# Optimization experiments

Measured on AMD Instinct MI355X. Metric: run time of the kernel, lower is better.

Reference implementation:

```python
import math
import jax, jax.numpy as jnp
import numpy as np

DIM, NHEAD, TOPK = 1024, 16, 64
DK = DIM // NHEAD
HIDDEN = int(DIM * 8.0)
EPS = 1e-5


def setup_inputs() -> dict:
    key = jax.random.key(0)
    ks = jax.random.split(key, 12)
    B, T = 2, 2048
    s = 0.02
    return {
        "x": jax.random.normal(ks[0], (B, T, DIM), jnp.float32),
        "ln1_g": jnp.ones((DIM,), jnp.float32),
        "ln1_b": jnp.zeros((DIM,), jnp.float32),
        "w_qkv": jax.random.normal(ks[1], (DIM, 3 * DIM), jnp.float32) * s,
        "alpha_head": jnp.zeros((NHEAD,), jnp.float32),
        "w_out": jax.random.normal(ks[2], (DIM, DIM), jnp.float32) * s,
        "ln2_g": jnp.ones((DIM,), jnp.float32),
        "ln2_b": jnp.zeros((DIM,), jnp.float32),
        "w1": jax.random.normal(ks[3], (DIM, HIDDEN), jnp.float32) * s,
        "b1": jnp.zeros((HIDDEN,), jnp.float32),
        "w2": jax.random.normal(ks[4], (HIDDEN, DIM), jnp.float32) * s,
        "b2": jnp.zeros((DIM,), jnp.float32),
        "alpha": jnp.float32(0.5),
    }


def _layernorm(x, g, b):
    mu = jnp.mean(x, axis=-1, keepdims=True)
    var = jnp.var(x, axis=-1, keepdims=True)
    return (x - mu) * jax.lax.rsqrt(var + EPS) * g + b


def _adaptive_sparse_attn(xn, w_qkv, alpha_head, w_out):
    B, T, C = xn.shape
    qkv = xn @ w_qkv  # [B,T,3C]
    q, k, v = jnp.split(qkv, 3, axis=-1)
    def heads(t):
        return t.reshape(B, T, NHEAD, DK).transpose(0, 2, 1, 3)  # [B,H,T,dk]
    q, k, v = heads(q), heads(k), heads(v)
    attn = jnp.einsum("bhqd,bhkd->bhqk", q, k) / math.sqrt(DK)  # [B,H,T,T]
    dense = jnp.einsum("bhqk,bhkd->bhqd", jax.nn.softmax(attn, axis=-1), v)
    # top-k sparse branch (TOPK < T)
    _, idx = jax.lax.top_k(attn, TOPK)  # [B,H,T,TOPK]
    M = B * NHEAD * T
    keep = jnp.zeros((M, T), bool).at[jnp.arange(M)[:, None], idx.reshape(M, TOPK)].set(True)
    keep = keep.reshape(B, NHEAD, T, T)
    attn_sp = jnp.where(keep, attn, jnp.float32(-1e9))
    sparse = jnp.einsum("bhqk,bhkd->bhqd", jax.nn.softmax(attn_sp, axis=-1), v)
    gate = jax.nn.sigmoid(alpha_head)[None, :, None, None]
    out = gate * dense + (1.0 - gate) * sparse  # [B,H,T,dk]
    out = out.transpose(0, 2, 1, 3).reshape(B, T, C)
    return out @ w_out


def reference(x, ln1_g, ln1_b, w_qkv, alpha_head, w_out, ln2_g, ln2_b, w1, b1, w2, b2, alpha):
    # attention sub-block with learned residual scale alpha
    x = x + alpha * _adaptive_sparse_attn(_layernorm(x, ln1_g, ln1_b), w_qkv, alpha_head, w_out)
    # FFN (dropout in eval mode -> identity); exact GELU as torch default
    h = jax.nn.gelu(_layernorm(x, ln2_g, ln2_b) @ w1 + b1, approximate=False)
    x = x + alpha * (h @ w2 + b2)
    return x
```

## Files before the change

### kernel.cpp

```cpp
#include <hip/hip_runtime.h>
#include <hip/hip_bf16.h>
#include <math.h>

#define DIMC 1024
#define NHEADC 16
#define DKC 64
#define HIDC 8192
#define TSEQ 2048
#define BATCH 2
#define NROWS (BATCH*TSEQ)
#define EPSF 1e-5f

typedef __attribute__((ext_vector_type(8))) short short8;
typedef __attribute__((ext_vector_type(4))) float floatx4;

__device__ __forceinline__ unsigned pk2bf(float a, float b){
  float2 t; t.x = a; t.y = b;
  __hip_bfloat162 h = __float22bfloat162_rn(t);
  union { __hip_bfloat162 h; unsigned u; } cv; cv.h = h;
  return cv.u;
}
__device__ __forceinline__ ushort f2bf(float f){
  return (ushort)(pk2bf(f, f) & 0xFFFFu);
}
__device__ __forceinline__ floatx4 mfma16(short8 a, short8 b, floatx4 c){
  return __builtin_amdgcn_mfma_f32_16x16x32_bf16(a, b, c, 0, 0, 0);
}
__device__ __forceinline__ void gld_lds16(const void* g, void* l){
  __builtin_amdgcn_global_load_lds((const __attribute__((address_space(1))) unsigned*)g,
                                   (__attribute__((address_space(3))) unsigned*)l, 16, 0, 0);
}
__device__ __forceinline__ float wred_add(float v){
  #pragma unroll
  for (int o = 32; o > 0; o >>= 1) v += __shfl_xor(v, o, 64);
  return v;
}
__device__ __forceinline__ int wred_addi(int v){
  #pragma unroll
  for (int o = 32; o > 0; o >>= 1) v += __shfl_xor(v, o, 64);
  return v;
}
__device__ __forceinline__ unsigned wred_maxu(unsigned v){
  #pragma unroll
  for (int o = 32; o > 0; o >>= 1) { unsigned w = __shfl_xor((int)v, o, 64); v = v > w ? v : w; }
  return v;
}
__device__ __forceinline__ unsigned wred_minu(unsigned v){
  #pragma unroll
  for (int o = 32; o > 0; o >>= 1) { unsigned w = __shfl_xor((int)v, o, 64); v = v < w ? v : w; }
  return v;
}
__device__ __forceinline__ float lo16f(unsigned u){ return __uint_as_float(u << 16); }
__device__ __forceinline__ float hi16f(unsigned u){ return __uint_as_float(u & 0xFFFF0000u); }
__device__ __forceinline__ unsigned pk2key(unsigned u){
  const unsigned s = u & 0x80008000u;
  return u ^ (0x80008000u | (s - (s >> 15)));
}
__device__ __forceinline__ unsigned key2pk(unsigned k){
  const unsigned s = k & 0x80008000u;
  return k ^ ~(s - (s >> 15));
}

__global__ __launch_bounds__(256)
void wconv_t(const float* __restrict__ W, ushort* __restrict__ WT, int K, int N)
{
  __shared__ float tile[32][33];
  const int t = threadIdx.x, tx = t & 31, ty = t >> 5;
  const int n0 = blockIdx.x * 32, k0 = blockIdx.y * 32;
  #pragma unroll
  for (int r = 0; r < 4; ++r)
    tile[ty + r*8][tx] = W[(size_t)(k0 + ty + r*8) * N + n0 + tx];
  __syncthreads();
  #pragma unroll
  for (int r = 0; r < 4; ++r)
    WT[(size_t)(n0 + ty + r*8) * K + k0 + tx] = f2bf(tile[tx][ty + r*8]);
}

__global__ __launch_bounds__(256)
void vtrans(const ushort* __restrict__ qkv, ushort* __restrict__ vT)
{
  const int d = threadIdx.x & 63, tp = threadIdx.x >> 6;
  const int bh = blockIdx.y; const int h = bh & 15, b = bh >> 4;
  const int t0 = blockIdx.x * 32 + tp * 8;
  const ushort* src = qkv + ((size_t)(b*TSEQ) + t0) * (3*DIMC) + 2*DIMC + h*DKC + d;
  ushort tmp[8];
  #pragma unroll
  for (int k = 0; k < 8; ++k) tmp[k] = src[(size_t)k * (3*DIMC)];
  *(short8*)&vT[((size_t)bh*DKC + d)*TSEQ + t0] = *(const short8*)tmp;
}

__global__ __launch_bounds__(256)
void ln_bf16(const float* __restrict__ x, const float* __restrict__ g,
             const float* __restrict__ b, ushort* __restrict__ y)
{
  __shared__ float red[8];
  const int row = blockIdx.x;
  const float* xr = x + (size_t)row * DIMC;
  const int c = threadIdx.x * 4;
  float4 v = *(const float4*)&xr[c];
  float s  = v.x + v.y + v.z + v.w;
  float ss = v.x*v.x + v.y*v.y + v.z*v.z + v.w*v.w;
  s = wred_add(s); ss = wred_add(ss);
  const int warp = threadIdx.x >> 6, lane = threadIdx.x & 63;
  if (lane == 0) { red[warp] = s; red[4+warp] = ss; }
  __syncthreads();
  s  = red[0] + red[1] + red[2] + red[3];
  ss = red[4] + red[5] + red[6] + red[7];
  const float mu  = s  * (1.f/DIMC);
  const float var = ss * (1.f/DIMC) - mu*mu;
  const float rr  = rsqrtf(var + EPSF);
  const float4 gv = *(const float4*)&g[c];
  const float4 bv = *(const float4*)&b[c];
  uint2 o;
  o.x = pk2bf((v.x-mu)*rr*gv.x + bv.x, (v.y-mu)*rr*gv.y + bv.y);
  o.y = pk2bf((v.z-mu)*rr*gv.z + bv.z, (v.w-mu)*rr*gv.w + bv.w);
  *(uint2*)&y[(size_t)row*DIMC + c] = o;
}

#define M_PLAIN 0
#define M_RES 1
#define M_BIAS_GELU 2
#define M_BIAS_RES 3

template<int MODE>
__global__ __launch_bounds__(256)
void gemm_bf16(const ushort* __restrict__ A, const ushort* __restrict__ BT,
               void* __restrict__ Cout, const int M, const int N, const int K,
               const float* __restrict__ bias, const float* __restrict__ res,
               const float* __restrict__ alphap)
{
  __shared__ __align__(16) ushort Al[4][128][8];
  __shared__ __align__(16) ushort Bl[4][128][8];
  const int t = threadIdx.x;
  const int lane = t & 63, warp = t >> 6;
  const int quad = lane >> 4, l16 = lane & 15;
  const int m0 = (warp & 1) * 64, n0 = (warp >> 1) * 64;
  const size_t row0 = (size_t)blockIdx.y * 128;
  const size_t col0 = (size_t)blockIdx.x * 128;

  const int c0 = t, c1 = t + 256;
  const int ar0 = c0 & 127, as0 = c0 >> 7;
  const int ar1 = c1 & 127, as1 = c1 >> 7;
  const ushort* pa0 = A  + (row0 + ar0) * (size_t)K + as0 * 8;
  const ushort* pa1 = A  + (row0 + ar1) * (size_t)K + as1 * 8;
  const ushort* pb0 = BT + (col0 + ar0) * (size_t)K + as0 * 8;
  const ushort* pb1 = BT + (col0 + ar1) * (size_t)K + as1 * 8;
  ushort* la0 = &Al[as0][ar0][0];
  ushort* la1 = &Al[as1][ar1][0];
  ushort* lb0 = &Bl[as0][ar0][0];
  ushort* lb1 = &Bl[as1][ar1][0];

  floatx4 acc[4][4];
  const floatx4 zf = {0.f, 0.f, 0.f, 0.f};
  #pragma unroll
  for (int i = 0; i < 4; ++i)
    #pragma unroll
    for (int j = 0; j < 4; ++j) acc[i][j] = zf;

  for (int k0 = 0; k0 < K; k0 += 32) {
    gld_lds16(pa0 + k0, la0);
    gld_lds16(pa1 + k0, la1);
    gld_lds16(pb0 + k0, lb0);
    gld_lds16(pb1 + k0, lb1);
    __syncthreads();
    short8 af[4], bfr[4];
    #pragma unroll
    for (int i = 0; i < 4; ++i) {
      af[i]  = *(const short8*)&Al[quad][m0 + i*16 + l16][0];
      bfr[i] = *(const short8*)&Bl[quad][n0 + i*16 + l16][0];
    }
    #pragma unroll
    for (int mt = 0; mt < 4; ++mt)
      #pragma unroll
      for (int nt = 0; nt < 4; ++nt)
        acc[mt][nt] = mfma16(af[mt], bfr[nt], acc[mt][nt]);
    __syncthreads();
  }

  float alpha = 0.f;
  if (MODE == M_RES || MODE == M_BIAS_RES) alpha = alphap[0];
  #pragma unroll
  for (int nt = 0; nt < 4; ++nt) {
    const size_t col = col0 + n0 + nt*16 + l16;
    float bv = 0.f;
    if (MODE == M_BIAS_GELU || MODE == M_BIAS_RES) bv = bias[col];
    #pragma unroll
    for (int mt = 0; mt < 4; ++mt) {
      const size_t r0 = row0 + m0 + mt*16 + quad*4;
      #pragma unroll
      for (int reg = 0; reg < 4; ++reg) {
        float v = acc[mt][nt][reg];
        if (MODE == M_BIAS_GELU || MODE == M_BIAS_RES) v += bv;
        if (MODE == M_BIAS_GELU) v = 0.5f*v*(1.f + erff(v*0.70710678118654752f));
        if (MODE == M_RES || MODE == M_BIAS_RES) v = res[(r0+reg)*(size_t)N + col] + alpha*v;
        if (MODE == M_PLAIN || MODE == M_BIAS_GELU)
          ((ushort*)Cout)[(r0+reg)*(size_t)N + col] = f2bf(v);
        else
          ((float*)Cout)[(r0+reg)*(size_t)N + col] = v;
      }
    }
  }
}

__device__ __forceinline__ int swzf(int q){ return ((q>>2) ^ q) & 7; }
__device__ __forceinline__ int sidx(int q, int j){
  return (q << 11) + ((((j >> 3) ^ swzf(q)) << 3) | (j & 7));
}

__global__ __launch_bounds__(1024, 8)
void attn_mfma(const ushort* __restrict__ qkv, const ushort* __restrict__ vT,
               const float* __restrict__ alpha_head, ushort* __restrict__ att)
{
  __shared__ __align__(16) ushort S[16*2048];
  __shared__ float Ored[3][4][16*17];
  const int t = threadIdx.x;
  const int lane = t & 63, warp = t >> 6;
  const int quad = lane >> 4, l16 = lane & 15;
  const int blk = blockIdx.x;
  const int bh  = blk >> 7;
  const int q0  = (blk & 127) << 4;
  const int h = bh & (NHEADC-1), b = bh >> 4;
  const size_t rowbase = (size_t)b * TSEQ;
  const floatx4 zf = {0.f, 0.f, 0.f, 0.f};

  {
    const ushort* Qp = qkv + (rowbase + q0 + l16) * (size_t)(3*DIMC) + h*DKC + quad*8;
    const short8 aq0 = *(const short8*)Qp;
    const short8 aq1 = *(const short8*)(Qp + 32);
    const int j0w = warp * 128;
    #pragma unroll
    for (int jt = 0; jt < 8; ++jt) {
      const int j = j0w + jt*16;
      const ushort* Kp = qkv + (rowbase + j + l16) * (size_t)(3*DIMC) + DIMC + h*DKC + quad*8;
      const short8 kb0 = *(const short8*)Kp;
      const short8 kb1 = *(const short8*)(Kp + 32);
      floatx4 c = mfma16(aq0, kb0, zf);
      c = mfma16(aq1, kb1, c);
      #pragma unroll
      for (int r = 0; r < 4; ++r)
        S[sidx(quad*4 + r, j + l16)] = f2bf(c[r]);
    }
  }
  __syncthreads();

  const float SC2 = 0.125f * 1.4426950408889634f;
  const float gate = 1.f / (1.f + __expf(-alpha_head[h]));
  {
    const int q = warp;
    const int sbase = q << 11;
    const int swq = swzf(q);
    const int a0 = sbase + 8*(((lane >> 1) ^ swq)) + 4*(lane & 1);

    unsigned lmxk = 0u;
    #pragma unroll
    for (int p = 0; p < 8; ++p) {
      uint2 w = *(const uint2*)&S[a0 + 256*p];
      const unsigned k0 = pk2key(w.x), k1 = pk2key(w.y);
      w.x = k0; w.y = k1;
      *(uint2*)&S[a0 + 256*p] = w;
      unsigned m0 = (k0 & 0xFFFFu) > (k0 >> 16) ? (k0 & 0xFFFFu) : (k0 >> 16);
      unsigned m1 = (k1 & 0xFFFFu) > (k1 >> 16) ? (k1 & 0xFFFFu) : (k1 >> 16);
      m0 = m0 > m1 ? m0 : m1;
      lmxk = lmxk > m0 ? lmxk : m0;
    }
    const unsigned kmx = wred_maxu(lmxk);
    const unsigned klb = wred_minu(lmxk);
    const unsigned mb = (kmx >= 0x8000u) ? (kmx - 0x8000u) : (0xFFFFu - kmx);
    const float nc = -__uint_as_float(mb << 16) * SC2;

    const unsigned diff = kmx ^ klb;
    unsigned prefix;
    int hb;
    if (diff == 0u) { prefix = kmx; hb = -1; }
    else {
      hb = 31 - __builtin_clz(diff);
      prefix = kmx & ~((2u << hb) - 1u);
    }
    hb = __builtin_amdgcn_readfirstlane(hb);
    for (int bit = hb; bit >= 0; --bit) {
      const int cand = (int)(prefix | (1u << bit));
      int c = 32;
      #pragma unroll
      for (int p = 0; p < 8; ++p) {
        const uint2 w = *(const uint2*)&S[a0 + 256*p];
        c += ((int)(w.x & 0xFFFFu) - cand) >> 31;
        c += ((int)(w.x >> 16)     - cand) >> 31;
        c += ((int)(w.y & 0xFFFFu) - cand) >> 31;
        c += ((int)(w.y >> 16)     - cand) >> 31;
      }
      c = wred_addi(c);
      prefix = (c >= 64) ? (unsigned)cand : prefix;
    }

    const int pfx = (int)prefix;
    unsigned inmask = 0u, eqmask = 0u;
    int cg = 0;
    #pragma unroll
    for (int p = 0; p < 8; ++p) {
      const uint2 w = *(const uint2*)&S[a0 + 256*p];
      const unsigned k0 = w.x & 0xFFFFu, k1 = w.x >> 16;
      const unsigned k2 = w.y & 0xFFFFu, k3 = w.y >> 16;
      const unsigned g0 = (unsigned)((pfx - (int)k0) >> 31) & 1u;
      const unsigned g1 = (unsigned)((pfx - (int)k1) >> 31) & 1u;
      const unsigned g2 = (unsigned)((pfx - (int)k2) >> 31) & 1u;
      const unsigned g3 = (unsigned)((pfx - (int)k3) >> 31) & 1u;
      cg += (int)(g0 + g1 + g2 + g3);
      inmask |= (g0 << (4*p)) | (g1 << (4*p+1)) | (g2 << (4*p+2)) | (g3 << (4*p+3));
      eqmask |= ((unsigned)(k0 == prefix) << (4*p))   | ((unsigned)(k1 == prefix) << (4*p+1))
              | ((unsigned)(k2 == prefix) << (4*p+2)) | ((unsigned)(k3 == prefix) << (4*p+3));
    }
    const int c_gt = wred_addi(cg);
    const int need_eq = 64 - c_gt;

    int eqb = 0;
    const unsigned long long below = (1ULL << lane) - 1ULL;
    #pragma unroll
    for (int p = 0; p < 8; ++p) {
      const bool e0 = (eqmask >> (4*p))   & 1u;
      const bool e1 = (eqmask >> (4*p+1)) & 1u;
      const bool e2 = (eqmask >> (4*p+2)) & 1u;
      const bool e3 = (eqmask >> (4*p+3)) & 1u;
      const unsigned long long m0 = __ballot(e0);
      const unsigned long long m1 = __ballot(e1);
      const unsigned long long m2 = __ballot(e2);
      const unsigned long long m3 = __ballot(e3);
      if (m0 | m1 | m2 | m3) {
        int r = eqb + __popcll(m0 & below) + __popcll(m1 & below)
                    + __popcll(m2 & below) + __popcll(m3 & below);
        if (e0) { if (r < need_eq) inmask |= 1u << (4*p);   ++r; }
        if (e1) { if (r < need_eq) inmask |= 1u << (4*p+1); ++r; }
        if (e2) { if (r < need_eq) inmask |= 1u << (4*p+2); ++r; }
        if (e3) { if (r < need_eq) inmask |= 1u << (4*p+3); ++r; }
        eqb += __popcll(m0) + __popcll(m1) + __popcll(m2) + __popcll(m3);
      }
    }

    float sum_all = 0.f, sum_sp = 0.f;
    #pragma unroll
    for (int p = 0; p < 8; ++p) {
      const uint2 w = *(const uint2*)&S[a0 + 256*p];
      const unsigned s0 = key2pk(w.x), s1 = key2pk(w.y);
      const float e0 = exp2f(fmaf(lo16f(s0), SC2, nc));
      const float e1 = exp2f(fmaf(hi16f(s0), SC2, nc));
      const float e2 = exp2f(fmaf(lo16f(s1), SC2, nc));
      const float e3 = exp2f(fmaf(hi16f(s1), SC2, nc));
      sum_all += (e0 + e1) + (e2 + e3);
      sum_sp  += ((inmask >> (4*p))   & 1u) ? e0 : 0.f;
      sum_sp  += ((inmask >> (4*p+1)) & 1u) ? e1 : 0.f;
      sum_sp  += ((inmask >> (4*p+2)) & 1u) ? e2 : 0.f;
      sum_sp  += ((inmask >> (4*p+3)) & 1u) ? e3 : 0.f;
    }
    sum_all = wred_add(sum_all);
    sum_sp  = wred_add(sum_sp);

    const float cd  = gate / sum_all;
    const float cdc = cd + (1.f - gate) / sum_sp;
    #pragma unroll
    for (int p = 0; p < 8; ++p) {
      uint2 w = *(const uint2*)&S[a0 + 256*p];
      const unsigned s0 = key2pk(w.x), s1 = key2pk(w.y);
      const float e0 = exp2f(fmaf(lo16f(s0), SC2, nc));
      const float e1 = exp2f(fmaf(hi16f(s0), SC2, nc));
      const float e2 = exp2f(fmaf(lo16f(s1), SC2, nc));
      const float e3 = exp2f(fmaf(hi16f(s1), SC2, nc));
      const float w0 = e0 * (((inmask >> (4*p))   & 1u) ? cdc : cd);
      const float w1 = e1 * (((inmask >> (4*p+1)) & 1u) ? cdc : cd);
      const float w2 = e2 * (((inmask >> (4*p+2)) & 1u) ? cdc : cd);
      const float w3 = e3 * (((inmask >> (4*p+3)) & 1u) ? cdc : cd);
      w.x = pk2bf(w0, w1);
      w.y = pk2bf(w2, w3);
      *(uint2*)&S[a0 + 256*p] = w;
    }
  }
  __syncthreads();

  const int ng = warp & 3, kq = warp >> 2;
  const int n0  = ng * 16;
  const int kt0 = kq * 16;
  floatx4 o = zf, o2 = zf;
  const ushort* Vb = vT + ((size_t)bh*DKC + n0 + l16) * TSEQ + quad*8;
  #pragma unroll 2
  for (int tt = 0; tt < 16; tt += 2) {
    const int kt = kt0 + tt;
    const short8 a0v = *(const short8*)&S[sidx(l16, kt*32 + quad*8)];
    const short8 vb0 = *(const short8*)(Vb + (size_t)kt*32);
    const short8 a1v = *(const short8*)&S[sidx(l16, (kt+1)*32 + quad*8)];
    const short8 vb1 = *(const short8*)(Vb + (size_t)(kt+1)*32);
    o  = mfma16(a0v, vb0, o);
    o2 = mfma16(a1v, vb1, o2);
  }
  o = o + o2;
  if (kq > 0) {
    #pragma unroll
    for (int r = 0; r < 4; ++r) Ored[kq-1][ng][(quad*4+r)*17 + l16] = o[r];
  }
  __syncthreads();
  if (kq == 0) {
    #pragma unroll
    for (int r = 0; r < 4; ++r) {
      const int ri = (quad*4+r)*17 + l16;
      const float v = o[r] + Ored[0][ng][ri] + Ored[1][ng][ri] + Ored[2][ng][ri];
      att[(rowbase + q0 + quad*4 + r) * (size_t)DIMC + h*DKC + n0 + l16] = f2bf(v);
    }
  }
}

extern "C" void kernel_launch(void* const* d_in, const int* in_sizes, int n_in,
                              void* d_out, int out_size, void* d_ws, size_t ws_size,
                              hipStream_t stream)
{
  const float* x          = (const float*)d_in[0];
  const float* ln1_g      = (const float*)d_in[1];
  const float* ln1_b      = (const float*)d_in[2];
  const float* w_qkv      = (const float*)d_in[3];
  const float* alpha_head = (const float*)d_in[4];
  const float* w_out      = (const float*)d_in[5];
  const float* ln2_g      = (const float*)d_in[6];
  const float* ln2_b      = (const float*)d_in[7];
  const float* w1         = (const float*)d_in[8];
  const float* b1         = (const float*)d_in[9];
  const float* w2         = (const float*)d_in[10];
  const float* b2         = (const float*)d_in[11];
  const float* alphap     = (const float*)d_in[12];
  float* out = (float*)d_out;

  char* ws = (char*)d_ws;
  ushort* wT_qkv = (ushort*)(ws);
  ushort* wT_out = (ushort*)(ws + 6291456);
  ushort* wT_1   = (ushort*)(ws + 8388608);
  ushort* wT_2   = (ushort*)(ws + 25165824);
  ushort* xn     = (ushort*)(ws + 41943040);
  ushort* qkv    = (ushort*)(ws + 50331648);
  ushort* attb   = (ushort*)(ws + 75497472);
  float*  x2     = (float*) (ws + 83886080);
  ushort* hbuf   = (ushort*)(ws + 100663296);
  ushort* vT     = (ushort*)(ws + 167772160);

  wconv_t<<<dim3(3072/32, 1024/32), 256, 0, stream>>>(w_qkv, wT_qkv, 1024, 3072);
  wconv_t<<<dim3(1024/32, 1024/32), 256, 0, stream>>>(w_out, wT_out, 1024, 1024);
  wconv_t<<<dim3(8192/32, 1024/32), 256, 0, stream>>>(w1,    wT_1,   1024, 8192);
  wconv_t<<<dim3(1024/32, 8192/32), 256, 0, stream>>>(w2,    wT_2,   8192, 1024);

  ln_bf16<<<NROWS, 256, 0, stream>>>(x, ln1_g, ln1_b, xn);
  gemm_bf16<M_PLAIN><<<dim3(3*DIMC/128, NROWS/128), 256, 0, stream>>>(
      xn, wT_qkv, qkv, NROWS, 3*DIMC, DIMC, nullptr, nullptr, nullptr);
  vtrans<<<dim3(64, 32), 256, 0, stream>>>(qkv, vT);
  attn_mfma<<<4096, 1024, 0, stream>>>(qkv, vT, alpha_head, attb);
  gemm_bf16<M_RES><<<dim3(DIMC/128, NROWS/128), 256, 0, stream>>>(
      attb, wT_out, x2, NROWS, DIMC, DIMC, nullptr, x, alphap);
  ln_bf16<<<NROWS, 256, 0, stream>>>(x2, ln2_g, ln2_b, xn);
  gemm_bf16<M_BIAS_GELU><<<dim3(HIDC/128, NROWS/128), 256, 0, stream>>>(
      xn, wT_1, hbuf, NROWS, HIDC, DIMC, b1, nullptr, nullptr);
  gemm_bf16<M_BIAS_RES><<<dim3(DIMC/128, NROWS/128), 256, 0, stream>>>(
      hbuf, wT_2, out, NROWS, DIMC, HIDC, b2, x2, alphap);
}
```

Baseline: 986.0 us.

## Split-K the output projection and FFN down GEMMs with a combine kernel

The out-projection and FFN second GEMM each launched only 8x32=256 blocks with long K loops, so the GPU's compute units were underfilled. They now run as split-K with two slices along blockIdx.z. Each slice writes fp32 partial sums to a workspace buffer that reuses the xn/qkv region. A new combine2 kernel adds the two partials plus bias, scales by alpha and adds the residual. This buys more parallelism at the cost of extra fp32 partial traffic (two 16MB writes and reads per GEMM) and two extra launches.

```diff
diff --git a/kernel.cpp b/kernel.cpp
--- a/kernel.cpp
+++ b/kernel.cpp
@@ -121,13 +121,14 @@
 #define M_RES 1
 #define M_BIAS_GELU 2
 #define M_BIAS_RES 3
+#define M_PARTIAL 4
 
 template<int MODE>
 __global__ __launch_bounds__(256)
 void gemm_bf16(const ushort* __restrict__ A, const ushort* __restrict__ BT,
                void* __restrict__ Cout, const int M, const int N, const int K,
                const float* __restrict__ bias, const float* __restrict__ res,
-               const float* __restrict__ alphap)
+               const float* __restrict__ alphap, const int ldk)
 {
   __shared__ __align__(16) ushort Al[4][128][8];
   __shared__ __align__(16) ushort Bl[4][128][8];
@@ -137,14 +138,16 @@
   const int m0 = (warp & 1) * 64, n0 = (warp >> 1) * 64;
   const size_t row0 = (size_t)blockIdx.y * 128;
   const size_t col0 = (size_t)blockIdx.x * 128;
+  const ushort* Ab = A  + (size_t)blockIdx.z * K;
+  const ushort* Bb = BT + (size_t)blockIdx.z * K;
 
   const int c0 = t, c1 = t + 256;
   const int ar0 = c0 & 127, as0 = c0 >> 7;
   const int ar1 = c1 & 127, as1 = c1 >> 7;
-  const ushort* pa0 = A  + (row0 + ar0) * (size_t)K + as0 * 8;
-  const ushort* pa1 = A  + (row0 + ar1) * (size_t)K + as1 * 8;
-  const ushort* pb0 = BT + (col0 + ar0) * (size_t)K + as0 * 8;
-  const ushort* pb1 = BT + (col0 + ar1) * (size_t)K + as1 * 8;
+  const ushort* pa0 = Ab + (row0 + ar0) * (size_t)ldk + as0 * 8;
+  const ushort* pa1 = Ab + (row0 + ar1) * (size_t)ldk + as1 * 8;
+  const ushort* pb0 = Bb + (col0 + ar0) * (size_t)ldk + as0 * 8;
+  const ushort* pb1 = Bb + (col0 + ar1) * (size_t)ldk + as1 * 8;
   ushort* la0 = &Al[as0][ar0][0];
   ushort* la1 = &Al[as1][ar1][0];
   ushort* lb0 = &Bl[as0][ar0][0];
@@ -179,6 +182,7 @@
 
   float alpha = 0.f;
   if (MODE == M_RES || MODE == M_BIAS_RES) alpha = alphap[0];
+  const size_t zoff = (MODE == M_PARTIAL) ? (size_t)blockIdx.z * M * N : 0;
   #pragma unroll
   for (int nt = 0; nt < 4; ++nt) {
     const size_t col = col0 + n0 + nt*16 + l16;
@@ -196,10 +200,32 @@
         if (MODE == M_PLAIN || MODE == M_BIAS_GELU)
           ((ushort*)Cout)[(r0+reg)*(size_t)N + col] = f2bf(v);
         else
-          ((float*)Cout)[(r0+reg)*(size_t)N + col] = v;
+          ((float*)Cout)[zoff + (r0+reg)*(size_t)N + col] = v;
       }
     }
   }
+}
+
+template<bool HB>
+__global__ __launch_bounds__(256)
+void combine2(const float* __restrict__ p, const float* __restrict__ res,
+              const float* __restrict__ bias, const float* __restrict__ alphap,
+              float* __restrict__ out)
+{
+  const int c = threadIdx.x * 4;
+  const size_t i = (size_t)blockIdx.x * DIMC + c;
+  const float alpha = alphap[0];
+  const float4 a = *(const float4*)&p[i];
+  const float4 b = *(const float4*)&p[(size_t)NROWS * DIMC + i];
+  const float4 r = *(const float4*)&res[i];
+  float bx = 0.f, by = 0.f, bz = 0.f, bw = 0.f;
+  if (HB) { const float4 bv = *(const float4*)&bias[c]; bx = bv.x; by = bv.y; bz = bv.z; bw = bv.w; }
+  float4 o;
+  o.x = r.x + alpha * (a.x + b.x + bx);
+  o.y = r.y + alpha * (a.y + b.y + by);
+  o.z = r.z + alpha * (a.z + b.z + bz);
+  o.w = r.w + alpha * (a.w + b.w + bw);
+  *(float4*)&out[i] = o;
 }
 
 __device__ __forceinline__ int swzf(int q){ return ((q>>2) ^ q) & 7; }
@@ -435,6 +461,7 @@
   float*  x2     = (float*) (ws + 83886080);
   ushort* hbuf   = (ushort*)(ws + 100663296);
   ushort* vT     = (ushort*)(ws + 167772160);
+  float*  part   = (float*) (ws + 41943040);
 
   wconv_t<<<dim3(3072/32, 1024/32), 256, 0, stream>>>(w_qkv, wT_qkv, 1024, 3072);
   wconv_t<<<dim3(1024/32, 1024/32), 256, 0, stream>>>(w_out, wT_out, 1024, 1024);
@@ -443,14 +470,16 @@
 
   ln_bf16<<<NROWS, 256, 0, stream>>>(x, ln1_g, ln1_b, xn);
   gemm_bf16<M_PLAIN><<<dim3(3*DIMC/128, NROWS/128), 256, 0, stream>>>(
-      xn, wT_qkv, qkv, NROWS, 3*DIMC, DIMC, nullptr, nullptr, nullptr);
+      xn, wT_qkv, qkv, NROWS, 3*DIMC, DIMC, nullptr, nullptr, nullptr, DIMC);
   vtrans<<<dim3(64, 32), 256, 0, stream>>>(qkv, vT);
   attn_mfma<<<4096, 1024, 0, stream>>>(qkv, vT, alpha_head, attb);
-  gemm_bf16<M_RES><<<dim3(DIMC/128, NROWS/128), 256, 0, stream>>>(
-      attb, wT_out, x2, NROWS, DIMC, DIMC, nullptr, x, alphap);
+  gemm_bf16<M_PARTIAL><<<dim3(DIMC/128, NROWS/128, 2), 256, 0, stream>>>(
+      attb, wT_out, part, NROWS, DIMC, DIMC/2, nullptr, nullptr, nullptr, DIMC);
+  combine2<false><<<NROWS, 256, 0, stream>>>(part, x, nullptr, alphap, x2);
   ln_bf16<<<NROWS, 256, 0, stream>>>(x2, ln2_g, ln2_b, xn);
   gemm_bf16<M_BIAS_GELU><<<dim3(HIDC/128, NROWS/128), 256, 0, stream>>>(
-      xn, wT_1, hbuf, NROWS, HIDC, DIMC, b1, nullptr, nullptr);
-  gemm_bf16<M_BIAS_RES><<<dim3(DIMC/128, NROWS/128), 256, 0, stream>>>(
-      hbuf, wT_2, out, NROWS, DIMC, HIDC, b2, x2, alphap);
-}
+      xn, wT_1, hbuf, NROWS, HIDC, DIMC, b1, nullptr, nullptr, DIMC);
+  gemm_bf16<M_PARTIAL><<<dim3(DIMC/128, NROWS/128, 2), 256, 0, stream>>>(
+      hbuf, wT_2, part, NROWS, DIMC, HIDC/2, nullptr, nullptr, nullptr, HIDC);
+  combine2<true><<<NROWS, 256, 0, stream>>>(part, x2, b2, alphap, out);
+}
```

Result: faster. 911.2 us (-7.6%).
